# Kernel tuning notes

Measured on AMD Instinct MI355X. Metric: run time of the kernel, lower is better.

The kernel has to match this reference:

```python
import jax, jax.numpy as jnp
import numpy as np

CLIP_LIMIT = 40.0
GRID = (8, 8)
NUM_BINS = 256


def setup_inputs() -> dict:
    key = jax.random.key(0)
    img = jax.random.uniform(key, (32, 3, 512, 512), dtype=jnp.float32)
    return {"img": img}


def _axis_map(n, T, G):
    # For each pixel coordinate along one axis: the two neighboring tile
    # indices (t0, t1) and the linear blend weight for t0 (kornia CLAHE scheme:
    # interpolation blocks span tile-center to tile-center; border half-tiles
    # use a single LUT, i.e. t0 == t1, w == 1).
    pos = jnp.arange(n)
    r = pos - T // 2
    inside = (pos >= T // 2) & (pos < (G - 1) * T + T // 2)
    k = jnp.clip(r // T, 0, G - 2)
    t0 = jnp.where(inside, k, jnp.where(pos < T // 2, 0, G - 1))
    t1 = jnp.where(inside, jnp.minimum(k + 1, G - 1), t0)
    rr = r - k * T  # row within the interpolation block, in [0, T)
    w = jnp.where(inside, (T - 1 - rr).astype(jnp.float32) / (T - 1.0), 1.0)
    return t0, t1, w


def _clahe(img):
    B, C, H, W = img.shape
    GH, GW = GRID
    TH, TW = H // GH, W // GW  # H, W chosen divisible (even tiles, no padding)
    pixels = TH * TW
    nb = NUM_BINS

    # ---- per-tile histograms (torch.histc: 256 bins over [0,1]) ----
    bin_idx = jnp.clip(jnp.floor(img * nb).astype(jnp.int32), 0, nb - 1)  # B,C,H,W
    ty_tile = (jnp.arange(H) // TH)[None, None, :, None]
    tx_tile = (jnp.arange(W) // TW)[None, None, None, :]
    b_i = jnp.arange(B)[:, None, None, None]
    c_i = jnp.arange(C)[None, :, None, None]
    # segment id ordered as (B, GH, GW, C, bin) to match the LUT layout below
    seg = (((b_i * GH + ty_tile) * GW + tx_tile) * C + c_i) * nb + bin_idx
    N = B * GH * GW * C
    hist = jax.ops.segment_sum(
        jnp.ones((B * C * H * W,), jnp.float32), seg.ravel(), num_segments=N * nb
    ).reshape(N, nb)

    # ---- clip + redistribute excess (kornia _compute_luts) ----
    if CLIP_LIMIT > 0.0:
        max_val = max(CLIP_LIMIT * pixels // nb, 1.0)
        hist = jnp.minimum(hist, max_val)
        excess = pixels - hist.sum(axis=1)
        residual = jnp.remainder(excess, nb)
        redist = (excess - residual) / nb
        hist = hist + redist[:, None]
        hist = hist + (jnp.arange(nb)[None, :] < residual[:, None]).astype(hist.dtype)

    # ---- CDF -> LUT (scale by 255/pixels, clamp, floor) ----
    luts = jnp.floor(jnp.clip(jnp.cumsum(hist, axis=1) * ((nb - 1) / pixels), 0, nb - 1))
    luts = luts.reshape(B, GH, GW, C, nb)

    # ---- bilinear blend of the 4 neighboring tile LUTs per pixel ----
    ty0, ty1, wy = _axis_map(H, TH, GH)
    tx0, tx1, wx = _axis_map(W, TW, GW)
    v = jnp.clip(jnp.floor(img * (nb - 1)).astype(jnp.int32), 0, nb - 1)  # B,C,H,W

    def gather(t_y, t_x):
        # luts[b, t_y[y], t_x[x], c, v[b,c,y,x]] -> (B,C,H,W)
        return luts[b_i, t_y[None, None, :, None], t_x[None, None, None, :], c_i, v]

    wy_ = wy[None, None, :, None]
    wx_ = wx[None, None, None, :]
    out = (
        (wy_ * wx_) * gather(ty0, tx0)
        + (wy_ * (1.0 - wx_)) * gather(ty0, tx1)
        + ((1.0 - wy_) * wx_) * gather(ty1, tx0)
        + ((1.0 - wy_) * (1.0 - wx_)) * gather(ty1, tx1)
    )
    return out / (nb - 1.0)


def reference(img) -> jnp.ndarray:
    return _clahe(img)
```

## Files before the change

kernel.cpp:

```cpp
#include <hip/hip_runtime.h>


#define NBINS  256
#define TILE   64
#define CH     3
#define HH     512
#define WW     512
#define CLIPV  640
#define PIXELS 4096

#define LUTS_FLOATS (32 * 8 * 8 * 3 * NBINS)
#define V8_BYTES    ((size_t)32 * 3 * HH * WW)

typedef float f32x4 __attribute__((ext_vector_type(4)));

__global__ __launch_bounds__(256) void clahe_hist_lut_stripe(const float* __restrict__ img,
                                                             float* __restrict__ luts,
                                                             unsigned char* __restrict__ v8,
                                                             int write_v8) {
    const int t     = threadIdx.x;
    const int bid   = blockIdx.x;
    const int ty    = bid & 7;
    const int plane = bid >> 3;
    const int c     = plane % 3;
    const int bb    = plane / 3;

    __shared__ unsigned int hist[8][NBINS];
    #pragma unroll
    for (int h = 0; h < 8; ++h) hist[h][t] = 0u;
    __syncthreads();

    const size_t base = ((size_t)plane * HH + (size_t)ty * TILE) * WW;
    const f32x4* __restrict__ src  = reinterpret_cast<const f32x4*>(img + base);
    uchar4*      __restrict__ dst8 = reinterpret_cast<uchar4*>(v8 + base);

    #pragma unroll 4
    for (int it = 0; it < 32; ++it) {
        const int f = it * 256 + t;
        const f32x4 v = src[f];
        const int tile = (f & 127) >> 4;
        atomicAdd(&hist[tile][min(max((int)floorf(v.x * 256.0f), 0), 255)], 1u);
        atomicAdd(&hist[tile][min(max((int)floorf(v.y * 256.0f), 0), 255)], 1u);
        atomicAdd(&hist[tile][min(max((int)floorf(v.z * 256.0f), 0), 255)], 1u);
        atomicAdd(&hist[tile][min(max((int)floorf(v.w * 256.0f), 0), 255)], 1u);
        if (write_v8) {
            uchar4 q;
            q.x = (unsigned char)min(max((int)floorf(v.x * 255.0f), 0), 255);
            q.y = (unsigned char)min(max((int)floorf(v.y * 255.0f), 0), 255);
            q.z = (unsigned char)min(max((int)floorf(v.z * 255.0f), 0), 255);
            q.w = (unsigned char)min(max((int)floorf(v.w * 255.0f), 0), 255);
            dst8[f] = q;
        }
    }
    __syncthreads();

    const int lane = t & 63;
    const int wid  = t >> 6;

    #pragma unroll
    for (int s = 0; s < 2; ++s) {
        const int h = wid * 2 + s;
        int carry = 0;
        int incl[4];
        #pragma unroll
        for (int ch = 0; ch < 4; ++ch) {
            int v = min((int)hist[h][ch * 64 + lane], CLIPV);
            #pragma unroll
            for (int off = 1; off < 64; off <<= 1) {
                int n = __shfl_up(v, off, 64);
                if (lane >= off) v += n;
            }
            incl[ch] = carry + v;
            carry += __shfl(v, 63, 64);
        }
        const int total    = carry;
        const int excess   = PIXELS - total;
        const int residual = excess & 255;
        const int redist   = excess >> 8;
        const int job = ((bb * 8 + ty) * 8 + h) * 3 + c;
        float* __restrict__ dst = luts + (size_t)job * NBINS;
        #pragma unroll
        for (int ch = 0; ch < 4; ++ch) {
            const int bin = ch * 64 + lane;
            const int cum = incl[ch] + redist * (bin + 1) + min(bin + 1, residual);
            dst[bin] = floorf(fminf((float)cum * (255.0f / 4096.0f), 255.0f));
        }
    }
}

template<bool USE_V8>
__global__ __launch_bounds__(256) void clahe_apply_band(const float* __restrict__ img,
                                                        const unsigned char* __restrict__ v8,
                                                        const float* __restrict__ luts,
                                                        float* __restrict__ out) {
    __shared__ unsigned int Pack[9][NBINS];

    const int t     = threadIdx.x;
    const int bid   = blockIdx.x;
    const int g     = bid & 15;
    const int plane = bid >> 4;
    const int c     = plane % 3;
    const int bb    = plane / 3;
    const int y0    = g * 32;

    int ty0, ty1;
    if (y0 < 32)        { ty0 = 0; ty1 = 0; }
    else if (y0 >= 480) { ty0 = 7; ty1 = 7; }
    else                { ty0 = (y0 - 32) >> 6; ty1 = ty0 + 1; }

    const int rb0 = (bb * 8 + ty0) * 8;
    const int rb1 = (bb * 8 + ty1) * 8;

    int iL0[8], iL1[8];
    #pragma unroll
    for (int tx = 0; tx < 8; ++tx) {
        iL0[tx] = (int)luts[((size_t)((rb0 + tx) * 3 + c)) * NBINS + t];
        iL1[tx] = (int)luts[((size_t)((rb1 + tx) * 3 + c)) * NBINS + t];
    }
    #pragma unroll
    for (int tx = 0; tx < 8; ++tx) {
        int txn = (tx < 7) ? tx + 1 : 7;
        Pack[tx][t] = (unsigned)(iL1[tx] | (iL1[txn] << 8) | (iL0[tx] << 16) | (iL0[txn] << 24));
    }
    Pack[8][t] = (unsigned)(iL1[0] | (iL1[0] << 8) | (iL0[0] << 16) | (iL0[0] << 24));
    __syncthreads();

    const int x4f = t & 127;
    const int x   = x4f * 4;
    const int tx_sel = (x < 32) ? 8 : ((x >= 480) ? 7 : ((x - 32) >> 6));
    const unsigned int* __restrict__ Row = &Pack[tx_sel][0];
    float wxv[4];
    #pragma unroll
    for (int i = 0; i < 4; ++i) {
        const int xx = x + i;
        wxv[i] = (xx < 32 || xx >= 480) ? 1.0f
               : (float)(63 - ((xx - 32) & 63)) * (1.0f / 63.0f);
    }

    const size_t pb = (((size_t)plane) << 18) + (size_t)y0 * WW;
    const unsigned int* __restrict__ v8w = reinterpret_cast<const unsigned int*>(v8 + pb);
    const f32x4* __restrict__ imgw = reinterpret_cast<const f32x4*>(img + pb);
    f32x4* __restrict__ outw = reinterpret_cast<f32x4*>(out + pb);

    #pragma unroll 4
    for (int it = 0; it < 16; ++it) {
        const int fi  = it * 256 + t;
        const int row = fi >> 7;
        const int y   = y0 + row;
        const float wy = (float)(63 - ((y - 32) & 63)) * (1.0f / 63.0f);

        unsigned int w;
        float pix[4];
        if constexpr (USE_V8) {
            w = v8w[fi];
        } else {
            f32x4 f = imgw[fi];
            pix[0] = f.x; pix[1] = f.y; pix[2] = f.z; pix[3] = f.w;
        }

        f32x4 res;
        #pragma unroll
        for (int i = 0; i < 4; ++i) {
            int vv;
            if constexpr (USE_V8) vv = (w >> (8 * i)) & 255;
            else                  vv = min(max((int)floorf(pix[i] * 255.0f), 0), 255);
            const unsigned int raw = Row[vv];
            const float l1a = (float)(raw & 255u);
            const float l1b = (float)((raw >> 8) & 255u);
            const float l0a = (float)((raw >> 16) & 255u);
            const float l0b = (float)(raw >> 24);
            const float r0 = fmaf(wy, l0a - l1a, l1a);
            const float r1 = fmaf(wy, l0b - l1b, l1b);
            res[i] = fmaf(wxv[i], r0 - r1, r1) * (1.0f / 255.0f);
        }
        outw[fi] = res;
    }
}

extern "C" void kernel_launch(void* const* d_in, const int* in_sizes, int n_in,
                              void* d_out, int out_size, void* d_ws, size_t ws_size,
                              hipStream_t stream) {
    const float* img  = (const float*)d_in[0];
    float*       out  = (float*)d_out;
    float*       luts = (float*)d_ws;
    unsigned char* v8 = (unsigned char*)d_ws + (size_t)LUTS_FLOATS * 4;

    const bool use_v8 = ws_size >= (size_t)LUTS_FLOATS * 4 + V8_BYTES;

    clahe_hist_lut_stripe<<<768, 256, 0, stream>>>(img, luts, v8, use_v8 ? 1 : 0);
    if (use_v8)
        clahe_apply_band<true><<<1536, 256, 0, stream>>>(img, v8, luts, out);
    else
        clahe_apply_band<false><<<1536, 256, 0, stream>>>(img, v8, luts, out);
}
```

Baseline: 50.27 us.

## Fuse histogram/LUT and apply passes into one cooperative kernel with grid sync

```diff
diff --git a/kernel.cpp b/kernel.cpp
--- a/kernel.cpp
+++ b/kernel.cpp
@@ -1,4 +1,7 @@
 #include <hip/hip_runtime.h>
+#include <hip/hip_cooperative_groups.h>
+
+namespace cg = cooperative_groups;
 
 
 #define NBINS  256
@@ -13,6 +16,148 @@
 #define V8_BYTES    ((size_t)32 * 3 * HH * WW)
 
 typedef float f32x4 __attribute__((ext_vector_type(4)));
+
+__global__ __launch_bounds__(256) void clahe_fused2(const float* __restrict__ img,
+                                                    float* __restrict__ luts,
+                                                    unsigned char* __restrict__ v8,
+                                                    float* __restrict__ out) {
+    __shared__ unsigned int lds[9 * NBINS];
+
+    const int t     = threadIdx.x;
+    const int bid   = blockIdx.x;
+    const int ty    = bid & 7;
+    const int plane = bid >> 3;
+    const int c     = plane % 3;
+    const int bb    = plane / 3;
+
+    #pragma unroll
+    for (int h = 0; h < 8; ++h) lds[h * NBINS + t] = 0u;
+    __syncthreads();
+
+    const size_t base = ((size_t)plane * HH + (size_t)ty * TILE) * WW;
+    const f32x4* __restrict__ src  = reinterpret_cast<const f32x4*>(img + base);
+    uchar4*      __restrict__ dst8 = reinterpret_cast<uchar4*>(v8 + base);
+
+    #pragma unroll 4
+    for (int it = 0; it < 32; ++it) {
+        const int f = it * 256 + t;
+        const f32x4 v = src[f];
+        const int tile = (f & 127) >> 4;
+        atomicAdd(&lds[tile * NBINS + min(max((int)floorf(v.x * 256.0f), 0), 255)], 1u);
+        atomicAdd(&lds[tile * NBINS + min(max((int)floorf(v.y * 256.0f), 0), 255)], 1u);
+        atomicAdd(&lds[tile * NBINS + min(max((int)floorf(v.z * 256.0f), 0), 255)], 1u);
+        atomicAdd(&lds[tile * NBINS + min(max((int)floorf(v.w * 256.0f), 0), 255)], 1u);
+        uchar4 q;
+        q.x = (unsigned char)min(max((int)floorf(v.x * 255.0f), 0), 255);
+        q.y = (unsigned char)min(max((int)floorf(v.y * 255.0f), 0), 255);
+        q.z = (unsigned char)min(max((int)floorf(v.z * 255.0f), 0), 255);
+        q.w = (unsigned char)min(max((int)floorf(v.w * 255.0f), 0), 255);
+        dst8[f] = q;
+    }
+    __syncthreads();
+
+    const int lane = t & 63;
+    const int wid  = t >> 6;
+    #pragma unroll
+    for (int s = 0; s < 2; ++s) {
+        const int h = wid * 2 + s;
+        int carry = 0;
+        int incl[4];
+        #pragma unroll
+        for (int ch = 0; ch < 4; ++ch) {
+            int v = min((int)lds[h * NBINS + ch * 64 + lane], CLIPV);
+            #pragma unroll
+            for (int off = 1; off < 64; off <<= 1) {
+                int n = __shfl_up(v, off, 64);
+                if (lane >= off) v += n;
+            }
+            incl[ch] = carry + v;
+            carry += __shfl(v, 63, 64);
+        }
+        const int total    = carry;
+        const int excess   = PIXELS - total;
+        const int residual = excess & 255;
+        const int redist   = excess >> 8;
+        const int job = ((bb * 8 + ty) * 8 + h) * 3 + c;
+        float* __restrict__ dst = luts + (size_t)job * NBINS;
+        #pragma unroll
+        for (int ch = 0; ch < 4; ++ch) {
+            const int bin = ch * 64 + lane;
+            const int cum = incl[ch] + redist * (bin + 1) + min(bin + 1, residual);
+            dst[bin] = floorf(fminf((float)cum * (255.0f / 4096.0f), 255.0f));
+        }
+    }
+
+    __threadfence();
+    cg::this_grid().sync();
+
+    const unsigned int* __restrict__ v8w = reinterpret_cast<const unsigned int*>(v8 + base);
+    f32x4* __restrict__ outw = reinterpret_cast<f32x4*>(out + base);
+
+    const int x4f = t & 127;
+    const int x   = x4f * 4;
+    const int tx_sel = (x < 32) ? 8 : ((x >= 480) ? 7 : ((x - 32) >> 6));
+    const unsigned int* __restrict__ Row = &lds[tx_sel * NBINS];
+    float wxv[4];
+    #pragma unroll
+    for (int i = 0; i < 4; ++i) {
+        const int xx = x + i;
+        wxv[i] = (xx < 32 || xx >= 480) ? 1.0f
+               : (float)(63 - ((xx - 32) & 63)) * (1.0f / 63.0f);
+    }
+
+    #pragma unroll 1
+    for (int band = 0; band < 2; ++band) {
+        const int yb = ty * 64 + band * 32;
+        int ty0, ty1;
+        if (yb < 32)        { ty0 = 0; ty1 = 0; }
+        else if (yb >= 480) { ty0 = 7; ty1 = 7; }
+        else                { ty0 = (yb - 32) >> 6; ty1 = ty0 + 1; }
+        const int rb0 = (bb * 8 + ty0) * 8;
+        const int rb1 = (bb * 8 + ty1) * 8;
+
+        int iL0[8], iL1[8];
+        #pragma unroll
+        for (int tx = 0; tx < 8; ++tx) {
+            iL0[tx] = (int)luts[((size_t)((rb0 + tx) * 3 + c)) * NBINS + t];
+            iL1[tx] = (int)luts[((size_t)((rb1 + tx) * 3 + c)) * NBINS + t];
+        }
+        __syncthreads();
+        #pragma unroll
+        for (int tx = 0; tx < 8; ++tx) {
+            int txn = (tx < 7) ? tx + 1 : 7;
+            lds[tx * NBINS + t] = (unsigned)(iL1[tx] | (iL1[txn] << 8) |
+                                             (iL0[tx] << 16) | (iL0[txn] << 24));
+        }
+        lds[8 * NBINS + t] = (unsigned)(iL1[0] | (iL1[0] << 8) |
+                                        (iL0[0] << 16) | (iL0[0] << 24));
+        __syncthreads();
+
+        #pragma unroll 4
+        for (int it = band * 16; it < band * 16 + 16; ++it) {
+            const int fi  = it * 256 + t;
+            const int row = fi >> 7;
+            const int y   = ty * 64 + row;
+            const float wy = (float)(63 - ((y - 32) & 63)) * (1.0f / 63.0f);
+
+            const unsigned int w = v8w[fi];
+            f32x4 res;
+            #pragma unroll
+            for (int i = 0; i < 4; ++i) {
+                const int vv = (w >> (8 * i)) & 255;
+                const unsigned int raw = Row[vv];
+                const float l1a = (float)(raw & 255u);
+                const float l1b = (float)((raw >> 8) & 255u);
+                const float l0a = (float)((raw >> 16) & 255u);
+                const float l0b = (float)(raw >> 24);
+                const float r0 = fmaf(wy, l0a - l1a, l1a);
+                const float r1 = fmaf(wy, l0b - l1b, l1b);
+                res[i] = fmaf(wxv[i], r0 - r1, r1) * (1.0f / 255.0f);
+            }
+            outw[fi] = res;
+        }
+    }
+}
 
 __global__ __launch_bounds__(256) void clahe_hist_lut_stripe(const float* __restrict__ img,
                                                              float* __restrict__ luts,
@@ -56,7 +201,6 @@
 
     const int lane = t & 63;
     const int wid  = t >> 6;
-
     #pragma unroll
     for (int s = 0; s < 2; ++s) {
         const int h = wid * 2 + s;
@@ -187,9 +331,17 @@
 
     const bool use_v8 = ws_size >= (size_t)LUTS_FLOATS * 4 + V8_BYTES;
 
-    clahe_hist_lut_stripe<<<768, 256, 0, stream>>>(img, luts, v8, use_v8 ? 1 : 0);
-    if (use_v8)
-        clahe_apply_band<true><<<1536, 256, 0, stream>>>(img, v8, luts, out);
-    else
-        clahe_apply_band<false><<<1536, 256, 0, stream>>>(img, v8, luts, out);
+    hipError_t err = hipErrorUnknown;
+    if (use_v8) {
+        void* args[] = { (void*)&img, (void*)&luts, (void*)&v8, (void*)&out };
+        err = hipLaunchCooperativeKernel((const void*)clahe_fused2,
+                                         dim3(768), dim3(256), args, 0, stream);
+    }
+    if (err != hipSuccess) {
+        clahe_hist_lut_stripe<<<768, 256, 0, stream>>>(img, luts, v8, use_v8 ? 1 : 0);
+        if (use_v8)
+            clahe_apply_band<true><<<1536, 256, 0, stream>>>(img, v8, luts, out);
+        else
+            clahe_apply_band<false><<<1536, 256, 0, stream>>>(img, v8, luts, out);
+    }
 }
```

Measured after the change: 184.3 us. 3.67x slower.
